# Kernel optimization log

Measured on AMD Instinct MI355X. Metric: run time of the kernel, lower is better.

## Reference

```python
import jax, jax.numpy as jnp
import numpy as np

B, H, K, T, OUT, NH = 512, 512, 6, 60, 2, 8

def _gelu(x):
    return jax.nn.gelu(x, approximate=False)  # torch nn.GELU default = exact erf

def _layernorm(x, g, b, eps=1e-5):
    m = jnp.mean(x, axis=-1, keepdims=True)
    v = jnp.var(x, axis=-1, keepdims=True)
    return (x - m) * jax.lax.rsqrt(v + eps) * g + b

def setup_inputs() -> dict:
    key = jax.random.key(0)
    ks = iter(jax.random.split(key, 40))
    def p(shape, scale=0.02):
        return jax.random.normal(next(ks), shape, dtype=jnp.float32) * scale
    return dict(
        interaction_ctx=p((B, H), 1.0),
        cooperative_ctx=p((B, H), 1.0),
        map_ctx=p((B, H), 1.0),
        mode_queries=p((K, H)),
        # context_proj: Linear(3H,H) -> GELU -> Linear(H,H)
        Wc1=p((3 * H, H)), bc1=jnp.zeros((H,), jnp.float32),
        Wc2=p((H, H)), bc2=jnp.zeros((H,), jnp.float32),
        # coarse_heads stacked over modes: Linear(H,2H)->GELU->Linear(2H,T*OUT)
        Wk1=p((K, H, 2 * H)), bk1=jnp.zeros((K, 2 * H), jnp.float32),
        Wk2=p((K, 2 * H, T * OUT)), bk2=jnp.zeros((K, T * OUT), jnp.float32),
        # traj_encoder: Linear(OUT,H)->GELU
        Wt=p((OUT, H)), bt=jnp.zeros((H,), jnp.float32),
        # refine_attn (MultiheadAttention) projections
        Wq_a=p((H, H)), bq_a=jnp.zeros((H,), jnp.float32),
        Wk_a=p((H, H)), bk_a=jnp.zeros((H,), jnp.float32),
        Wv_a=p((H, H)), bv_a=jnp.zeros((H,), jnp.float32),
        Wo_a=p((H, H)), bo_a=jnp.zeros((H,), jnp.float32),
        ln_g=jnp.ones((H,), jnp.float32), ln_b=jnp.zeros((H,), jnp.float32),
        # refine_heads stacked over modes: Linear(H,H)->GELU->Linear(H,OUT)
        Wr1=p((K, H, H)), br1=jnp.zeros((K, H), jnp.float32),
        Wr2=p((K, H, OUT)), br2=jnp.zeros((K, OUT), jnp.float32),
        # conf_head: Linear(H,64)->ReLU->Linear(64,1)
        Wf1=p((H, 64)), bf1=jnp.zeros((64,), jnp.float32),
        Wf2=p((64, 1)), bf2=jnp.zeros((1,), jnp.float32),
    )

def reference(interaction_ctx, cooperative_ctx, map_ctx, mode_queries,
              Wc1, bc1, Wc2, bc2, Wk1, bk1, Wk2, bk2, Wt, bt,
              Wq_a, bq_a, Wk_a, bk_a, Wv_a, bv_a, Wo_a, bo_a,
              ln_g, ln_b, Wr1, br1, Wr2, br2, Wf1, bf1, Wf2, bf2):
    # dropout layers are identity in eval mode
    combined = jnp.concatenate([interaction_ctx, cooperative_ctx, map_ctx], axis=-1)  # (B,3H)
    context = _gelu(combined @ Wc1 + bc1) @ Wc2 + bc2                                 # (B,H)
    mode_features = mode_queries[None, :, :] + context[:, None, :]                    # (B,K,H)

    # coarse heads: per-mode loop -> grouped GEMM over mode axis
    h = _gelu(jnp.einsum('bkh,khf->bkf', mode_features, Wk1) + bk1)                   # (B,K,2H)
    coarse = (jnp.einsum('bkf,kfo->bko', h, Wk2) + bk2).reshape(B, K, T, OUT)          # (B,K,T,OUT)

    traj_feats = _gelu(coarse @ Wt + bt)                                              # (B,K,T,H)

    # refine_attn: keys/values are context broadcast over T (all identical), so
    # softmax weights are exactly uniform and attention output == out_proj(v_ctx).
    # (grads through Wq_a/Wk_a are exactly zero for the same reason.)
    v = context @ Wv_a + bv_a                                                         # (B,H)
    attn_out = v @ Wo_a + bo_a                                                        # (B,H)

    refined_feats = _layernorm(traj_feats + attn_out[:, None, None, :], ln_g, ln_b)   # (B,K,T,H)

    # refine heads: grouped GEMM over mode axis
    r = _gelu(jnp.einsum('bkth,khf->bktf', refined_feats, Wr1) + br1[:, None, :])     # (B,K,T,H)
    offsets = jnp.einsum('bktf,kfo->bkto', r, Wr2) + br2[:, None, :]                  # (B,K,T,OUT)
    predictions = coarse + offsets

    conf = jax.nn.relu(mode_features @ Wf1 + bf1) @ Wf2 + bf2                         # (B,K,1)
    mode_probs = jax.nn.softmax(conf[..., 0], axis=-1)                                # (B,K)
    return predictions, mode_probs
```

## Files before the change

kernel.cpp:

```cpp
#include <hip/hip_runtime.h>
#include <math.h>

#define BB 512
#define HH 512
#define KK 6
#define TT 60
#define OO 2
#define H2 1024
#define TO 120
#define RFP 520
#define HSP 1032

typedef __bf16 bf16x8 __attribute__((ext_vector_type(8)));
typedef float  f32x4  __attribute__((ext_vector_type(4)));
typedef float  f32x16 __attribute__((ext_vector_type(16)));

__device__ __forceinline__ float bf2f(unsigned short u) {
    union { unsigned int i; float f; } v; v.i = ((unsigned int)u) << 16; return v.f;
}
__device__ __forceinline__ unsigned short f2bf(float f) {
    union { float f; unsigned int i; } v; v.f = f;
    unsigned int b = v.i;
    return (unsigned short)((b + 0x7FFFu + ((b >> 16) & 1u)) >> 16);
}
__device__ __forceinline__ float gelu_exact(float x) {
    return 0.5f * x * (1.0f + erff(x * 0.70710678118654752f));
}

#if defined(__has_builtin)
#  if __has_builtin(__builtin_amdgcn_rcpf)
#    define FAST_RCP(x) __builtin_amdgcn_rcpf(x)
#  endif
#  if __has_builtin(__builtin_amdgcn_exp2f)
#    define FAST_EXP2(x) __builtin_amdgcn_exp2f(x)
#  endif
#endif
#ifndef FAST_RCP
#  define FAST_RCP(x) (1.0f / (x))
#endif
#ifndef FAST_EXP2
#  define FAST_EXP2(x) __expf((x) * 0.69314718056f)
#endif

__device__ __forceinline__ float gelu_cheap(float x) {
    float x2 = x * x;
    float z = x * fmaf(0.10294324f, x2, 2.3022082f);
    float e = FAST_EXP2(-z);
    return x * FAST_RCP(1.0f + e);
}

struct F8 { float v[8]; };
__device__ __forceinline__ F8 load8f(const float* p) {
    F8 r;
    float4 a = *(const float4*)p;
    float4 b = *(const float4*)(p + 4);
    r.v[0] = a.x; r.v[1] = a.y; r.v[2] = a.z; r.v[3] = a.w;
    r.v[4] = b.x; r.v[5] = b.y; r.v[6] = b.z; r.v[7] = b.w;
    return r;
}
__device__ __forceinline__ F8 load8b(const unsigned short* p) {
    ushort4 a = *(const ushort4*)p;
    ushort4 b = *(const ushort4*)(p + 4);
    F8 r;
    r.v[0] = bf2f(a.x); r.v[1] = bf2f(a.y); r.v[2] = bf2f(a.z); r.v[3] = bf2f(a.w);
    r.v[4] = bf2f(b.x); r.v[5] = bf2f(b.y); r.v[6] = bf2f(b.z); r.v[7] = bf2f(b.w);
    return r;
}

struct PKD { const float* src; unsigned short* dst; int F, N, NC, nch, steps, Z; };
struct PK8 { PKD e[8]; };

__global__ void k_pack(PK8 d) {
    int rid = blockIdx.x * 4 + (threadIdx.x >> 6);
    const int ln = threadIdx.x & 63;
    int i = 0;
    while (i < 7) {
        int tot = d.e[i].Z * d.e[i].nch * d.e[i].steps;
        if (rid < tot) break;
        rid -= tot; ++i;
    }
    const PKD e = d.e[i];
    const int per = e.nch * e.steps;
    const int z = rid / per;
    const int r = rid - z * per;
    const int nch = r / e.steps, step = r - nch * e.steps;
    const float* src = e.src + (size_t)z * e.F * e.N;
    unsigned short* dst = e.dst + ((size_t)z * per + r) * 512 + ln * 8;
    int f_base, n;
    if (e.NC == 16) { f_base = step * 32 + (ln >> 4) * 8; n = nch * 16 + (ln & 15); }
    else            { f_base = step * 16 + (ln >> 5) * 8; n = nch * 32 + (ln & 31); }
    if (n >= e.N) n = e.N - 1;
    unsigned int pk[4];
#pragma unroll
    for (int j = 0; j < 4; ++j) {
        unsigned short lo = f2bf(src[(size_t)(f_base + 2 * j) * e.N + n]);
        unsigned short hi = f2bf(src[(size_t)(f_base + 2 * j + 1) * e.N + n]);
        pk[j] = (unsigned int)lo | ((unsigned int)hi << 16);
    }
    *(uint4*)dst = make_uint4(pk[0], pk[1], pk[2], pk[3]);
}

template <bool CONCAT, bool GELU>
__launch_bounds__(256)
__global__ void k_gemm_m(const void* __restrict__ A0, const void* __restrict__ A1,
                         const void* __restrict__ A2, const unsigned short* __restrict__ BP,
                         const float* __restrict__ bias, unsigned short* __restrict__ C,
                         int Kd) {
    __shared__ __align__(16) unsigned short As[32 * RFP];
    const int tid = threadIdx.x;
    const int bm = blockIdx.x * 32;
    const int bn = blockIdx.y * 64;
    const int w = tid >> 6, ln = tid & 63;
    const int lane15 = ln & 15, quad = ln >> 4;
    const int n = bn + w * 16 + lane15;
    const int nchunks = Kd / HH;
    const int stepsTot = Kd / 32;
    const int nchB = blockIdx.y * 4 + w;

    f32x4 acc0 = {0.f, 0.f, 0.f, 0.f}, acc1 = {0.f, 0.f, 0.f, 0.f};

    for (int kc = 0; kc < nchunks; ++kc) {
        {
            int r = tid >> 3, c0 = (tid & 7) * 64;
            unsigned short* dp = As + r * RFP + c0;
            if (CONCAT) {
                const float* src = (kc == 0) ? (const float*)A0
                                 : (kc == 1) ? (const float*)A1 : (const float*)A2;
                const float* sp = src + (bm + r) * HH + c0;
                for (int c = 0; c < 64; c += 8) {
                    F8 v = load8f(sp + c);
                    unsigned int pk[4];
#pragma unroll
                    for (int j = 0; j < 4; ++j)
                        pk[j] = (unsigned int)f2bf(v.v[2 * j]) |
                                ((unsigned int)f2bf(v.v[2 * j + 1]) << 16);
                    *(uint4*)(dp + c) = make_uint4(pk[0], pk[1], pk[2], pk[3]);
                }
            } else {
                const unsigned short* sp = (const unsigned short*)A0 + (bm + r) * HH + c0;
                for (int c = 0; c < 64; c += 8)
                    *(uint4*)(dp + c) = *(const uint4*)(sp + c);
            }
        }
        __syncthreads();
        const unsigned short* bp = BP + ((size_t)nchB * stepsTot + kc * 16) * 512 + ln * 8;
#pragma unroll
        for (int f0 = 0; f0 < HH; f0 += 32) {
            bf16x8 a0 = *(const bf16x8*)(As + lane15 * RFP + f0 + quad * 8);
            bf16x8 a1 = *(const bf16x8*)(As + (16 + lane15) * RFP + f0 + quad * 8);
            bf16x8 bf = *(const bf16x8*)(bp);
            bp += 512;
            acc0 = __builtin_amdgcn_mfma_f32_16x16x32_bf16(a0, bf, acc0, 0, 0, 0);
            acc1 = __builtin_amdgcn_mfma_f32_16x16x32_bf16(a1, bf, acc1, 0, 0, 0);
        }
        __syncthreads();
    }
    const float bb = bias[n];
#pragma unroll
    for (int reg = 0; reg < 4; ++reg) {
        float v0 = acc0[reg] + bb, v1 = acc1[reg] + bb;
        if (GELU) { v0 = gelu_exact(v0); v1 = gelu_exact(v1); }
        C[(bm + quad * 4 + reg) * HH + n] = f2bf(v0);
        C[(bm + 16 + quad * 4 + reg) * HH + n] = f2bf(v1);
    }
}

__launch_bounds__(512)
__global__ void k_bc(const unsigned short* __restrict__ ctx, const float* __restrict__ mq,
                     const unsigned short* __restrict__ Wk1P, const float* __restrict__ bk1,
                     const unsigned short* __restrict__ Wk2P, const float* __restrict__ bk2,
                     const unsigned short* __restrict__ Wf1P, const float* __restrict__ bf1,
                     const float* __restrict__ Wf2, const float* __restrict__ bf2v,
                     unsigned short* __restrict__ coarse_out, float* __restrict__ conf_out)
{
    __shared__ __align__(16) unsigned short mf[16 * RFP];
    __shared__ __align__(16) unsigned short hs[16 * HSP];

    const int tid = threadIdx.x;
    const int k = blockIdx.x % KK;
    const int b0 = (blockIdx.x / KK) * 16;
    const int w = tid >> 6;
    const int ln = tid & 63;
    const int lane15 = ln & 15;
    const int quad = ln >> 4;

    {
        int r = tid >> 5;
        int c0 = (tid & 31) * 16;
        const unsigned short* cp = ctx + (b0 + r) * HH + c0;
        const float* qp = mq + k * HH + c0;
        unsigned short* dp = mf + r * RFP + c0;
        for (int c = 0; c < 16; c += 8) {
            F8 cv = load8b(cp + c);
            F8 qv = load8f(qp + c);
            unsigned int pk[4];
#pragma unroll
            for (int j = 0; j < 4; ++j)
                pk[j] = (unsigned int)f2bf(cv.v[2 * j] + qv.v[2 * j]) |
                        ((unsigned int)f2bf(cv.v[2 * j + 1] + qv.v[2 * j + 1]) << 16);
            *(uint4*)(dp + c) = make_uint4(pk[0], pk[1], pk[2], pk[3]);
        }
    }
    __syncthreads();

    {
        const unsigned short* wk1p = Wk1P + (size_t)k * (64 * 16 * 512);
        const float* bk1p = bk1 + k * H2;
        for (int g = 0; g < 8; ++g) {
            const int n = w * 128 + g * 16 + lane15;
            f32x4 acc0 = {0.f,0.f,0.f,0.f};
            const unsigned short* bp = wk1p + (size_t)((w * 8 + g) * 16) * 512 + ln * 8;
#pragma unroll
            for (int f0 = 0; f0 < HH; f0 += 32) {
                bf16x8 a0 = *(const bf16x8*)(mf + lane15 * RFP + f0 + quad * 8);
                bf16x8 bf = *(const bf16x8*)(bp);
                bp += 512;
                acc0 = __builtin_amdgcn_mfma_f32_16x16x32_bf16(a0, bf, acc0, 0, 0, 0);
            }
            const float bias = bk1p[n];
#pragma unroll
            for (int reg = 0; reg < 4; ++reg)
                hs[(quad * 4 + reg) * HSP + n] = f2bf(gelu_exact(acc0[reg] + bias));
        }
    }
    __syncthreads();

    {
        const unsigned short* wk2p = Wk2P + (size_t)k * (8 * 32 * 512);
        const int n = w * 16 + lane15;
        f32x4 acc0 = {0.f,0.f,0.f,0.f};
        const unsigned short* bp = wk2p + (size_t)(w * 32) * 512 + ln * 8;
#pragma unroll
        for (int f0 = 0; f0 < H2; f0 += 32) {
            bf16x8 a0 = *(const bf16x8*)(hs + lane15 * HSP + f0 + quad * 8);
            bf16x8 bf = *(const bf16x8*)(bp);
            bp += 512;
            acc0 = __builtin_amdgcn_mfma_f32_16x16x32_bf16(a0, bf, acc0, 0, 0, 0);
        }
        if (n < TO) {
            const float bias = bk2[k * TO + n];
#pragma unroll
            for (int reg = 0; reg < 4; ++reg)
                coarse_out[((b0 + quad * 4 + reg) * KK + k) * TO + n] = f2bf(acc0[reg] + bias);
        }
    }

    if (w == 0) {
        f32x4 acc[4];
#pragma unroll
        for (int nt = 0; nt < 4; ++nt) { f32x4 z = {0.f,0.f,0.f,0.f}; acc[nt] = z; }
#pragma unroll
        for (int f0 = 0; f0 < HH; f0 += 32) {
            const int step = f0 >> 5;
            bf16x8 a0 = *(const bf16x8*)(mf + lane15 * RFP + f0 + quad * 8);
#pragma unroll
            for (int nt = 0; nt < 4; ++nt) {
                bf16x8 bf = *(const bf16x8*)(Wf1P + (size_t)(nt * 16 + step) * 512 + ln * 8);
                acc[nt] = __builtin_amdgcn_mfma_f32_16x16x32_bf16(a0, bf, acc[nt], 0, 0, 0);
            }
        }
        const float b2 = bf2v[0];
#pragma unroll
        for (int reg = 0; reg < 4; ++reg) {
            float s = 0.f;
#pragma unroll
            for (int nt = 0; nt < 4; ++nt) {
                const int n = nt * 16 + lane15;
                s = fmaf(fmaxf(acc[nt][reg] + bf1[n], 0.f), Wf2[n], s);
            }
#pragma unroll
            for (int off = 1; off < 16; off <<= 1) s += __shfl_xor(s, off);
            if (lane15 == 0)
                conf_out[(b0 + quad * 4 + reg) * KK + k] = s + b2;
        }
    }
}

__launch_bounds__(512, 2)
__global__ void k_ef(
    const unsigned short* __restrict__ attn, const unsigned short* __restrict__ coarse_ws,
    const float* __restrict__ Wt,  const float* __restrict__ bt,
    const float* __restrict__ lng, const float* __restrict__ lnb,
    const unsigned short* __restrict__ Wr1P, const float* __restrict__ br1,
    const float* __restrict__ Wr2, const float* __restrict__ br2,
    float* __restrict__ pred_out)
{
    __shared__ __align__(16) unsigned short rf[2][64 * RFP];
    __shared__ float  po2[2][8][64][2];
    __shared__ float  br1d[2][HH];
    __shared__ float2 wr2d[2][HH];

    const int tid = threadIdx.x;
    const int b = blockIdx.x;
    const int w = tid >> 6;
    const int ln = tid & 63;
    const int lane31 = ln & 31;
    const int hf = ln >> 5;
    const int cbase = ln * 8;

    F8 w0 = load8f(Wt + cbase);
    F8 w1 = load8f(Wt + HH + cbase);
    F8 b8 = load8f(bt + cbase);
    F8 g8 = load8f(lng + cbase);
    F8 bb8 = load8f(lnb + cbase);
    F8 a8 = load8b(attn + b * HH + cbase);

    auto do_E = [&](int j, int buf) {
        unsigned short* rfb = &rf[buf][0];
        const unsigned short* cw = coarse_ws + (b * KK + j) * TO;
#pragma unroll
        for (int r = 0; r < 8; ++r) {
            int t = w + 8 * r;
            if (t < 60) {
                unsigned int cc = *(const unsigned int*)(cw + 2 * t);
                float co0 = bf2f((unsigned short)(cc & 0xffffu));
                float co1 = bf2f((unsigned short)(cc >> 16));
                float x[8]; float s = 0.f, s2 = 0.f;
#pragma unroll
                for (int jj = 0; jj < 8; ++jj) {
                    float vv = fmaf(co0, w0.v[jj], fmaf(co1, w1.v[jj], b8.v[jj]));
                    vv = gelu_cheap(vv) + a8.v[jj];
                    x[jj] = vv; s += vv; s2 = fmaf(vv, vv, s2);
                }
#pragma unroll
                for (int off = 32; off > 0; off >>= 1) {
                    s += __shfl_xor(s, off);
                    s2 += __shfl_xor(s2, off);
                }
                float mean = s * (1.0f / HH);
                float var = fmaf(-mean, mean, s2 * (1.0f / HH));
                float inv = rsqrtf(var + 1e-5f);
                unsigned int pk[4];
#pragma unroll
                for (int jj = 0; jj < 4; ++jj) {
                    float y0 = fmaf((x[2 * jj] - mean) * inv, g8.v[2 * jj], bb8.v[2 * jj]);
                    float y1 = fmaf((x[2 * jj + 1] - mean) * inv, g8.v[2 * jj + 1], bb8.v[2 * jj + 1]);
                    pk[jj] = (unsigned int)f2bf(y0) | ((unsigned int)f2bf(y1) << 16);
                }
                *(uint4*)(rfb + t * RFP + cbase) = make_uint4(pk[0], pk[1], pk[2], pk[3]);
            } else {
                *(uint4*)(rfb + t * RFP + cbase) = make_uint4(0, 0, 0, 0);
            }
        }
    };

    auto do_stage_g = [&](int j, int buf) {
        int i = tid & 255;
        br1d[buf][i]        = br1[j * HH + i];
        br1d[buf][i + 256]  = br1[j * HH + i + 256];
        wr2d[buf][i]        = ((const float2*)Wr2)[(size_t)j * HH + i];
        wr2d[buf][i + 256]  = ((const float2*)Wr2)[(size_t)j * HH + i + 256];
    };

    auto do_F = [&](int kk, int buf) {
        const unsigned short* bp0 = Wr1P + (size_t)kk * (16 * 32 * 512)
                                  + (size_t)(w * 2) * 32 * 512 + ln * 8;
        const unsigned short* bp1 = bp0 + 32 * 512;
        const int n0 = w * 64;
        const unsigned short* rfb = &rf[buf][0];
        const unsigned short* a0p = rfb + lane31 * RFP + hf * 8;
        const unsigned short* a1p = a0p + 32 * RFP;

        f32x16 acc00 = {0.f,0.f,0.f,0.f,0.f,0.f,0.f,0.f,0.f,0.f,0.f,0.f,0.f,0.f,0.f,0.f};
        f32x16 acc01 = acc00, acc10 = acc00, acc11 = acc00;

        __builtin_amdgcn_s_setprio(1);
#pragma unroll
        for (int st = 0; st < 32; ++st) {
            const int k0 = st * 16;
            bf16x8 A0 = *(const bf16x8*)(a0p + k0);
            bf16x8 A1 = *(const bf16x8*)(a1p + k0);
            bf16x8 B0 = *(const bf16x8*)(bp0 + st * 512);
            bf16x8 B1 = *(const bf16x8*)(bp1 + st * 512);
            acc00 = __builtin_amdgcn_mfma_f32_32x32x16_bf16(B0, A0, acc00, 0, 0, 0);
            acc01 = __builtin_amdgcn_mfma_f32_32x32x16_bf16(B1, A0, acc01, 0, 0, 0);
            acc10 = __builtin_amdgcn_mfma_f32_32x32x16_bf16(B0, A1, acc10, 0, 0, 0);
            acc11 = __builtin_amdgcn_mfma_f32_32x32x16_bf16(B1, A1, acc11, 0, 0, 0);
        }
        __builtin_amdgcn_s_setprio(0);

        float p00 = 0.f, p01 = 0.f, p10 = 0.f, p11 = 0.f;
#pragma unroll
        for (int nt = 0; nt < 2; ++nt) {
#pragma unroll
            for (int reg = 0; reg < 16; ++reg) {
                const int n = n0 + nt * 32 + (reg & 3) + 8 * (reg >> 2) + 4 * hf;
                const float bb = br1d[buf][n];
                const float2 w2 = wr2d[buf][n];
                const float a0v = nt ? acc01[reg] : acc00[reg];
                const float a1v = nt ? acc11[reg] : acc10[reg];
                const float rv0 = gelu_cheap(a0v + bb);
                const float rv1 = gelu_cheap(a1v + bb);
                p00 = fmaf(rv0, w2.x, p00);
                p01 = fmaf(rv0, w2.y, p01);
                p10 = fmaf(rv1, w2.x, p10);
                p11 = fmaf(rv1, w2.y, p11);
            }
        }
        p00 += __shfl_xor(p00, 32);
        p01 += __shfl_xor(p01, 32);
        p10 += __shfl_xor(p10, 32);
        p11 += __shfl_xor(p11, 32);
        if (ln < 32) {
            *(float2*)&po2[buf][w][lane31][0]      = make_float2(p00, p01);
            *(float2*)&po2[buf][w][32 + lane31][0] = make_float2(p10, p11);
        }
    };

    auto do_pred = [&](int kk, int buf) {
        if (tid < TO) {
            int t = tid >> 1, o = tid & 1;
            float s = 0.f;
#pragma unroll
            for (int ww = 0; ww < 8; ++ww) s += po2[buf][ww][t][o];
            float co = bf2f(coarse_ws[(b * KK + kk) * TO + tid]);
            pred_out[((b * KK + kk) * TT + t) * 2 + o] = co + s + br2[kk * 2 + o];
        }
    };

    {
        br1d[0][tid] = br1[tid];
        wr2d[0][tid] = ((const float2*)Wr2)[tid];
        do_E(0, 0);
    }
    __syncthreads();

    for (int kk = 0; kk < KK; ++kk) {
        const int cur = kk & 1;
        if (w < 4) {
            if (kk < KK - 1) { do_stage_g(kk + 1, cur ^ 1); do_E(kk + 1, cur ^ 1); }
            do_F(kk, cur);
        } else {
            do_F(kk, cur);
            if (kk < KK - 1) do_E(kk + 1, cur ^ 1);
        }
        __syncthreads();
        do_pred(kk, cur);
    }
}

__global__ void k_softmax(const float* __restrict__ conf, float* __restrict__ out) {
    int b = blockIdx.x * blockDim.x + threadIdx.x;
    if (b < BB) {
        float v[KK];
        float m = -1e30f;
        for (int i = 0; i < KK; ++i) { v[i] = conf[b * KK + i]; m = fmaxf(m, v[i]); }
        float s = 0.f;
        for (int i = 0; i < KK; ++i) { v[i] = __expf(v[i] - m); s += v[i]; }
        float inv = 1.0f / s;
        for (int i = 0; i < KK; ++i) out[b * KK + i] = v[i] * inv;
    }
}

extern "C" void kernel_launch(void* const* d_in, const int* in_sizes, int n_in,
                              void* d_out, int out_size, void* d_ws, size_t ws_size,
                              hipStream_t stream) {
    const float* I0  = (const float*)d_in[0];
    const float* I1  = (const float*)d_in[1];
    const float* I2  = (const float*)d_in[2];
    const float* MQ  = (const float*)d_in[3];
    const float* Wc1 = (const float*)d_in[4];
    const float* bc1 = (const float*)d_in[5];
    const float* Wc2 = (const float*)d_in[6];
    const float* bc2 = (const float*)d_in[7];
    const float* Wk1 = (const float*)d_in[8];
    const float* bk1 = (const float*)d_in[9];
    const float* Wk2 = (const float*)d_in[10];
    const float* bk2 = (const float*)d_in[11];
    const float* Wt  = (const float*)d_in[12];
    const float* bt  = (const float*)d_in[13];
    const float* Wv  = (const float*)d_in[18];
    const float* bv  = (const float*)d_in[19];
    const float* Wo  = (const float*)d_in[20];
    const float* bo  = (const float*)d_in[21];
    const float* lng = (const float*)d_in[22];
    const float* lnb = (const float*)d_in[23];
    const float* Wr1 = (const float*)d_in[24];
    const float* br1 = (const float*)d_in[25];
    const float* Wr2 = (const float*)d_in[26];
    const float* br2 = (const float*)d_in[27];
    const float* Wf1 = (const float*)d_in[28];
    const float* bf1 = (const float*)d_in[29];
    const float* Wf2 = (const float*)d_in[30];
    const float* bf2v = (const float*)d_in[31];

    unsigned short* wsu   = (unsigned short*)d_ws;
    unsigned short* wc1p  = wsu;
    unsigned short* wc2p  = wsu + 786432;
    unsigned short* wvp   = wsu + 1048576;
    unsigned short* wop   = wsu + 1310720;
    unsigned short* wk1p  = wsu + 1572864;
    unsigned short* wk2p  = wsu + 4718592;
    unsigned short* wf1p  = wsu + 5505024;
    unsigned short* wr1p  = wsu + 5537792;
    unsigned short* ctx   = wsu + 7110656;
    unsigned short* attn  = wsu + 7372800;
    unsigned short* tmp   = wsu + 7634944;
    unsigned short* coarse= wsu + 7897088;
    float* conf = (float*)(wsu + 8265728);

    float* pred = (float*)d_out;
    float* probs = pred + BB * KK * TT * OO;

    PK8 pk;
    pk.e[0] = {Wc1, wc1p, 3 * HH, HH, 16, 32, 48, 1};
    pk.e[1] = {Wc2, wc2p, HH, HH, 16, 32, 16, 1};
    pk.e[2] = {Wv,  wvp,  HH, HH, 16, 32, 16, 1};
    pk.e[3] = {Wo,  wop,  HH, HH, 16, 32, 16, 1};
    pk.e[4] = {Wk1, wk1p, HH, H2, 16, 64, 16, KK};
    pk.e[5] = {Wk2, wk2p, H2, TO, 16, 8, 32, KK};
    pk.e[6] = {Wf1, wf1p, HH, 64, 16, 4, 16, 1};
    pk.e[7] = {Wr1, wr1p, HH, HH, 32, 16, 32, KK};
    k_pack<<<dim3(3472), 256, 0, stream>>>(pk);

    k_gemm_m<true,  true ><<<dim3(16, 8), 256, 0, stream>>>(I0, I1, I2, wc1p, bc1, tmp, 3 * HH);
    k_gemm_m<false, false><<<dim3(16, 8), 256, 0, stream>>>(tmp, nullptr, nullptr, wc2p, bc2, ctx, HH);
    k_gemm_m<false, false><<<dim3(16, 8), 256, 0, stream>>>(ctx, nullptr, nullptr, wvp, bv, tmp, HH);
    k_gemm_m<false, false><<<dim3(16, 8), 256, 0, stream>>>(tmp, nullptr, nullptr, wop, bo, attn, HH);

    k_bc<<<dim3(192), 512, 0, stream>>>(ctx, MQ, wk1p, bk1, wk2p, bk2, wf1p, bf1, Wf2, bf2v,
                                        coarse, conf);
    k_ef<<<dim3(BB), 512, 0, stream>>>(attn, coarse, Wt, bt, lng, lnb,
                                       wr1p, br1, Wr2, br2, pred);
    k_softmax<<<dim3(2), 256, 0, stream>>>(conf, probs);
}
```

Before: 352.8 us.

## Warp-specialize k_ef into 8 MFMA waves and 8 producer waves

```diff
diff --git a/kernel.cpp b/kernel.cpp
--- a/kernel.cpp
+++ b/kernel.cpp
@@ -22,6 +22,11 @@
     union { float f; unsigned int i; } v; v.f = f;
     unsigned int b = v.i;
     return (unsigned short)((b + 0x7FFFu + ((b >> 16) & 1u)) >> 16);
+}
+__device__ __forceinline__ unsigned int pack2bf(float a, float b) {
+    union { __bf16 h[2]; unsigned int u; } v;
+    v.h[0] = (__bf16)a; v.h[1] = (__bf16)b;
+    return v.u;
 }
 __device__ __forceinline__ float gelu_exact(float x) {
     return 0.5f * x * (1.0f + erff(x * 0.70710678118654752f));
@@ -132,8 +137,7 @@
                     unsigned int pk[4];
 #pragma unroll
                     for (int j = 0; j < 4; ++j)
-                        pk[j] = (unsigned int)f2bf(v.v[2 * j]) |
-                                ((unsigned int)f2bf(v.v[2 * j + 1]) << 16);
+                        pk[j] = pack2bf(v.v[2 * j], v.v[2 * j + 1]);
                     *(uint4*)(dp + c) = make_uint4(pk[0], pk[1], pk[2], pk[3]);
                 }
             } else {
@@ -196,8 +200,7 @@
             unsigned int pk[4];
 #pragma unroll
             for (int j = 0; j < 4; ++j)
-                pk[j] = (unsigned int)f2bf(cv.v[2 * j] + qv.v[2 * j]) |
-                        ((unsigned int)f2bf(cv.v[2 * j + 1] + qv.v[2 * j + 1]) << 16);
+                pk[j] = pack2bf(cv.v[2 * j] + qv.v[2 * j], cv.v[2 * j + 1] + qv.v[2 * j + 1]);
             *(uint4*)(dp + c) = make_uint4(pk[0], pk[1], pk[2], pk[3]);
         }
     }
@@ -276,7 +279,7 @@
     }
 }
 
-__launch_bounds__(512, 2)
+__launch_bounds__(1024, 4)
 __global__ void k_ef(
     const unsigned short* __restrict__ attn, const unsigned short* __restrict__ coarse_ws,
     const float* __restrict__ Wt,  const float* __restrict__ bt,
@@ -297,20 +300,21 @@
     const int lane31 = ln & 31;
     const int hf = ln >> 5;
     const int cbase = ln * 8;
-
-    F8 w0 = load8f(Wt + cbase);
-    F8 w1 = load8f(Wt + HH + cbase);
-    F8 b8 = load8f(bt + cbase);
-    F8 g8 = load8f(lng + cbase);
-    F8 bb8 = load8f(lnb + cbase);
-    F8 a8 = load8b(attn + b * HH + cbase);
+    const int w8 = w & 7;
+    const bool fwave = (w < 8);
 
     auto do_E = [&](int j, int buf) {
+        F8 w0 = load8f(Wt + cbase);
+        F8 w1 = load8f(Wt + HH + cbase);
+        F8 b8 = load8f(bt + cbase);
+        F8 g8 = load8f(lng + cbase);
+        F8 bb8 = load8f(lnb + cbase);
+        F8 a8 = load8b(attn + b * HH + cbase);
         unsigned short* rfb = &rf[buf][0];
         const unsigned short* cw = coarse_ws + (b * KK + j) * TO;
 #pragma unroll
         for (int r = 0; r < 8; ++r) {
-            int t = w + 8 * r;
+            int t = w8 + 8 * r;
             if (t < 60) {
                 unsigned int cc = *(const unsigned int*)(cw + 2 * t);
                 float co0 = bf2f((unsigned short)(cc & 0xffffu));
@@ -335,7 +339,7 @@
                 for (int jj = 0; jj < 4; ++jj) {
                     float y0 = fmaf((x[2 * jj] - mean) * inv, g8.v[2 * jj], bb8.v[2 * jj]);
                     float y1 = fmaf((x[2 * jj + 1] - mean) * inv, g8.v[2 * jj + 1], bb8.v[2 * jj + 1]);
-                    pk[jj] = (unsigned int)f2bf(y0) | ((unsigned int)f2bf(y1) << 16);
+                    pk[jj] = pack2bf(y0, y1);
                 }
                 *(uint4*)(rfb + t * RFP + cbase) = make_uint4(pk[0], pk[1], pk[2], pk[3]);
             } else {
@@ -345,18 +349,16 @@
     };
 
     auto do_stage_g = [&](int j, int buf) {
-        int i = tid & 255;
-        br1d[buf][i]        = br1[j * HH + i];
-        br1d[buf][i + 256]  = br1[j * HH + i + 256];
-        wr2d[buf][i]        = ((const float2*)Wr2)[(size_t)j * HH + i];
-        wr2d[buf][i + 256]  = ((const float2*)Wr2)[(size_t)j * HH + i + 256];
+        int i = tid & 511;
+        br1d[buf][i] = br1[j * HH + i];
+        wr2d[buf][i] = ((const float2*)Wr2)[(size_t)j * HH + i];
     };
 
     auto do_F = [&](int kk, int buf) {
         const unsigned short* bp0 = Wr1P + (size_t)kk * (16 * 32 * 512)
-                                  + (size_t)(w * 2) * 32 * 512 + ln * 8;
+                                  + (size_t)(w8 * 2) * 32 * 512 + ln * 8;
         const unsigned short* bp1 = bp0 + 32 * 512;
-        const int n0 = w * 64;
+        const int n0 = w8 * 64;
         const unsigned short* rfb = &rf[buf][0];
         const unsigned short* a0p = rfb + lane31 * RFP + hf * 8;
         const unsigned short* a1p = a0p + 32 * RFP;
@@ -402,8 +404,8 @@
         p10 += __shfl_xor(p10, 32);
         p11 += __shfl_xor(p11, 32);
         if (ln < 32) {
-            *(float2*)&po2[buf][w][lane31][0]      = make_float2(p00, p01);
-            *(float2*)&po2[buf][w][32 + lane31][0] = make_float2(p10, p11);
+            *(float2*)&po2[buf][w8][lane31][0]      = make_float2(p00, p01);
+            *(float2*)&po2[buf][w8][32 + lane31][0] = make_float2(p10, p11);
         }
     };
 
@@ -418,21 +420,19 @@
         }
     };
 
-    {
-        br1d[0][tid] = br1[tid];
-        wr2d[0][tid] = ((const float2*)Wr2)[tid];
+    if (!fwave) {
+        do_stage_g(0, 0);
         do_E(0, 0);
     }
     __syncthreads();
 
     for (int kk = 0; kk < KK; ++kk) {
         const int cur = kk & 1;
-        if (w < 4) {
-            if (kk < KK - 1) { do_stage_g(kk + 1, cur ^ 1); do_E(kk + 1, cur ^ 1); }
+        if (fwave) {
             do_F(kk, cur);
-        } else {
-            do_F(kk, cur);
-            if (kk < KK - 1) do_E(kk + 1, cur ^ 1);
+        } else if (kk < KK - 1) {
+            do_stage_g(kk + 1, cur ^ 1);
+            do_E(kk + 1, cur ^ 1);
         }
         __syncthreads();
         do_pred(kk, cur);
@@ -520,7 +520,7 @@
 
     k_bc<<<dim3(192), 512, 0, stream>>>(ctx, MQ, wk1p, bk1, wk2p, bk2, wf1p, bf1, Wf2, bf2v,
                                         coarse, conf);
-    k_ef<<<dim3(BB), 512, 0, stream>>>(attn, coarse, Wt, bt, lng, lnb,
-                                       wr1p, br1, Wr2, br2, pred);
+    k_ef<<<dim3(BB), 1024, 0, stream>>>(attn, coarse, Wt, bt, lng, lnb,
+                                        wr1p, br1, Wr2, br2, pred);
     k_softmax<<<dim3(2), 256, 0, stream>>>(conf, probs);
 }
```

Result: slower. 380.8 us (+7.9%).
